# Kernel tuning notes

Hardware: AMD Instinct MI355X
Metric: run time of the kernel (lower is better)

The kernel has to match this reference:

```python
import jax, jax.numpy as jnp
import numpy as np

B, S, N, F, E, EF, H, L = 4, 16, 2048, 32, 16384, 8, 64, 2
H2 = H // 2


def setup_inputs() -> dict:
    key = jax.random.key(0)
    ks = iter(jax.random.split(key, 40))

    def g(shape, s=0.05):
        return jax.random.normal(next(ks), shape, jnp.float32) * s

    return dict(
        x=jax.random.normal(next(ks), (B, S, N, F), jnp.float32),
        edge_index=jax.random.randint(next(ks), (2, E), 0, N, dtype=jnp.int32),
        edge_attr=jax.random.normal(next(ks), (E, EF), jnp.float32),
        Wp=g((F, H)), bp=jnp.zeros((H,), jnp.float32),
        Wl=g((L, H, H)), bl=jnp.zeros((L, H), jnp.float32),
        Wr=g((L, H, H)), br=jnp.zeros((L, H), jnp.float32),
        We=g((L, EF, H)), att=g((L, H)), gb=jnp.zeros((L, H), jnp.float32),
        Wih=g((L, 3 * H, H)), Whh=g((L, 3 * H, H)),
        bih=jnp.zeros((L, 3 * H), jnp.float32), bhh=jnp.zeros((L, 3 * H), jnp.float32),
        oW1=g((H, H2)), ob1=jnp.zeros((H2,), jnp.float32),
        oW2=g((H2, 1)), ob2=jnp.zeros((1,), jnp.float32),
        dW1=g((H, H2)), db1=jnp.zeros((H2,), jnp.float32),
        dW2=g((H2, 1)), db2=jnp.zeros((1,), jnp.float32),
    )


def reference(x, edge_index, edge_attr, Wp, bp, Wl, bl, Wr, br, We, att, gb,
              Wih, Whh, bih, bhh, oW1, ob1, oW2, ob2, dW1, db1, dW2, db2):
    b, s, n, f = x.shape
    nl, _, h = Wl.shape
    src, dst = edge_index[0], edge_index[1]
    # GATv2Conv add_self_loops with fill_value='mean': self-loop attr = mean of
    # incoming edge attrs per destination node (0 if none).
    ones = jnp.ones((src.shape[0],), x.dtype)
    cnt = jax.ops.segment_sum(ones, dst, num_segments=n)
    loop_attr = jax.ops.segment_sum(edge_attr, dst, num_segments=n) / jnp.maximum(cnt, 1.0)[:, None]
    ar = jnp.arange(n, dtype=src.dtype)
    src_f = jnp.concatenate([src, ar])
    dst_f = jnp.concatenate([dst, ar])
    ea_f = jnp.concatenate([edge_attr, loop_attr], axis=0)  # [E2, EF]

    def gat(Xg, l):
        # Xg: [G, N, H] -- GATv2 (heads=1) applied independently per graph.
        XL = Xg @ Wl[l] + bl[l]
        XR = Xg @ Wr[l] + br[l]
        ep = ea_f @ We[l]                              # [E2, H]
        m = XL[:, src_f] + XR[:, dst_f] + ep[None]     # [G, E2, H]
        m = jax.nn.leaky_relu(m, 0.2)
        logits = m @ att[l]                            # [G, E2]
        seg_max = jax.vmap(lambda lg: jax.ops.segment_max(lg, dst_f, num_segments=n))(logits)
        p = jnp.exp(logits - seg_max[:, dst_f])
        den = jax.vmap(lambda pg: jax.ops.segment_sum(pg, dst_f, num_segments=n))(p)
        alpha = p / den[:, dst_f]
        out = jax.vmap(lambda a, xl: jax.ops.segment_sum(a[:, None] * xl[src_f], dst_f, num_segments=n))(alpha, XL)
        return out + gb[l]

    def gru(seq, l):
        # seq: [T, M, H]; PyTorch GRU gate order (r, z, n), scan over T.
        def step(hprev, xt):
            gi = xt @ Wih[l].T + bih[l]
            gh = hprev @ Whh[l].T + bhh[l]
            ir, iz, inn = jnp.split(gi, 3, -1)
            hr, hz, hn = jnp.split(gh, 3, -1)
            r = jax.nn.sigmoid(ir + hr)
            z = jax.nn.sigmoid(iz + hz)
            nn_ = jnp.tanh(inn + r * hn)
            hnew = (1.0 - z) * nn_ + z * hprev
            return hnew, hnew
        h0 = jnp.zeros(seq.shape[1:], seq.dtype)
        _, ys = jax.lax.scan(step, h0, seq)
        return ys

    X = x @ Wp + bp  # [B, S, N, H]
    for l in range(nl):
        # Original code applies GAT per (outer-t, inner-b) pair; the inner
        # TemporalGNN's GRU recurs over the BATCH axis (length B) per outer t.
        hg = gat(X.reshape(b * s, n, h), l).reshape(b, s, n, h)
        X = gru(hg.reshape(b, s * n, h), l).reshape(b, s, n, h)
    xl = X[:, -1].reshape(b * n, h)  # x[:, -1] then per-node heads, concat dim=1
    order = jax.nn.relu(xl @ oW1 + ob1) @ oW2 + ob2
    demand = jax.nn.relu(xl @ dW1 + db1) @ dW2 + db2
    return order[None], demand[None]  # each [1, B*N, 1]
```

## Files before the change

kernel.cpp:

```cpp
#include <hip/hip_runtime.h>
#include <math.h>

#define Bb   4
#define Ss   16
#define Nn   2048
#define Ff   32
#define Ee   16384
#define EFf  8
#define Hh   64
#define HB2  32
#define E2c  (Ee + Nn)
#define RTOT (Bb*Ss*Nn)
#define Mm   (Ss*Nn)
#define CST  68

typedef __attribute__((ext_vector_type(8))) short short8;
typedef __attribute__((ext_vector_type(4))) float f32x4;
#define MFMA16 __builtin_amdgcn_mfma_f32_16x16x32_bf16

__device__ __forceinline__ float sigf(float x) { return 1.f / (1.f + __expf(-x)); }
__device__ __forceinline__ float tanhfast(float x) { return 2.f / (1.f + __expf(-2.f * x)) - 1.f; }

__device__ __forceinline__ void split_bf16(float x, unsigned short& h, unsigned short& l) {
  unsigned u = __float_as_uint(x);
  unsigned r = (u + 0x7FFFu + ((u >> 16) & 1u)) >> 16;
  h = (unsigned short)r;
  float rest = x - __uint_as_float(r << 16);
  unsigned u2 = __float_as_uint(rest);
  l = (unsigned short)((u2 + 0x7FFFu + ((u2 >> 16) & 1u)) >> 16);
}

template <int PAT>
__device__ __forceinline__ float xorf(float v) {
  return __int_as_float(__builtin_amdgcn_ds_swizzle(__float_as_int(v), PAT));
}
__device__ __forceinline__ float red8(float v) {
  int x = __builtin_amdgcn_update_dpp(0, __float_as_int(v), 0x128, 0xF, 0xF, true);
  v += __int_as_float(x);
  v += xorf<0x401F>(v);
  v += __shfl_xor(v, 32, 64);
  return v;
}
__device__ __forceinline__ float redlogit(float v) {
  int x;
  x = __builtin_amdgcn_update_dpp(0, __float_as_int(v), 0xB1, 0xF, 0xF, true);
  v += __int_as_float(x);
  x = __builtin_amdgcn_update_dpp(0, __float_as_int(v), 0x4E, 0xF, 0xF, true);
  v += __int_as_float(x);
  v += xorf<0x101F>(v);
  return v;
}

__global__ __launch_bounds__(256) void k_loop_accum(
    const int* __restrict__ ei, const float* __restrict__ ea,
    float* __restrict__ cntF, float* __restrict__ loopA) {
  int idx = blockIdx.x * 256 + threadIdx.x;
  int e = idx >> 3, j = idx & 7;
  int d = ei[Ee + e];
  atomicAdd(&loopA[d * EFf + j], ea[idx]);
  if (j == 0) atomicAdd(&cntF[d], 1.0f);
}

__global__ __launch_bounds__(256) void k_scan(
    const float* __restrict__ cntF, int* __restrict__ offs) {
  __shared__ int partial[256];
  int tid = threadIdx.x;
  int base = tid * 8;
  int vals[8];
  int s = 0;
  for (int i = 0; i < 8; ++i) {
    int c = (int)cntF[base + i] + 1;
    vals[i] = c;
    s += c;
  }
  partial[tid] = s;
  __syncthreads();
  for (int off = 1; off < 256; off <<= 1) {
    int v = partial[tid];
    int add = (tid >= off) ? partial[tid - off] : 0;
    __syncthreads();
    partial[tid] = v + add;
    __syncthreads();
  }
  int run = (tid == 0) ? 0 : partial[tid - 1];
  for (int i = 0; i < 8; ++i) {
    offs[base + i] = run;
    run += vals[i];
  }
  if (tid == 255) offs[Nn] = run;
}

__global__ __launch_bounds__(256) void k_scatter(
    const int* __restrict__ ei, const int* __restrict__ offs,
    int* __restrict__ fillI, int* __restrict__ posOf, int* __restrict__ srcA) {
  int e = blockIdx.x * 256 + threadIdx.x;
  if (e >= E2c) return;
  int d = (e < Ee) ? ei[Ee + e] : (e - Ee);
  int s = (e < Ee) ? ei[e]      : (e - Ee);
  int pos = offs[d] + atomicAdd(&fillI[d], 1);
  posOf[e] = pos;
  srcA[pos] = s;
}

__global__ __launch_bounds__(256) void k_wprep(
    const float* __restrict__ Wl, const float* __restrict__ Wr,
    const float* __restrict__ Wih, const float* __restrict__ Whh,
    unsigned short* __restrict__ WXhi, unsigned short* __restrict__ WXlo,
    unsigned short* __restrict__ WGhi, unsigned short* __restrict__ WGlo) {
  int idx = blockIdx.x * 256 + threadIdx.x;
  if (idx < 16384) {
    int j = idx & 7, lane = (idx >> 3) & 63, kh = (idx >> 9) & 1;
    int t = (idx >> 10) & 7, l = idx >> 13;
    int n = t * 16 + (lane & 15);
    int k = kh * 32 + ((lane >> 4) << 3) + j;
    const float* W = (n < 64) ? (Wl + (size_t)l * 4096) : (Wr + (size_t)l * 4096);
    float v = W[k * 64 + (n & 63)];
    unsigned short h, lo;
    split_bf16(v, h, lo);
    WXhi[idx] = h; WXlo[idx] = lo;
  } else {
    int i2 = idx - 16384;
    int j = i2 & 7, lane = (i2 >> 3) & 63, kh = (i2 >> 9) & 1;
    int t = (i2 >> 10) % 24, l = i2 / 24576;
    int n = t * 16 + (lane & 15);
    int k = kh * 32 + ((lane >> 4) << 3) + j;
    int g = n >> 6, c = n & 63;
    const float* W = (g < 3) ? (Wih + (size_t)l * 12288 + (size_t)(g * 64 + c) * 64)
                             : (Whh + (size_t)l * 12288 + (size_t)((g - 3) * 64 + c) * 64);
    float v = W[k];
    unsigned short h, lo;
    split_bf16(v, h, lo);
    WGhi[i2] = h; WGlo[i2] = lo;
  }
}

__global__ __launch_bounds__(256) void k_ep(
    const float* __restrict__ ea, const float* __restrict__ loopA,
    const float* __restrict__ We, const int* __restrict__ posOf,
    const float* __restrict__ cntF, float* __restrict__ EPc) {
  __shared__ float wlds[EFf * Hh];
  int tid = threadIdx.x;
  int l = blockIdx.y;
  const float* Wel = We + (size_t)l * EFf * Hh;
  if (tid < EFf * Hh) wlds[tid] = Wel[tid];
  if (tid + 256 < EFf * Hh) wlds[tid + 256] = Wel[tid + 256];
  __syncthreads();
  int idx = blockIdx.x * 256 + tid;
  int e = idx >> 6, j = idx & 63;
  const float* a = (e < Ee) ? (ea + (size_t)e * EFf) : (loopA + (size_t)(e - Ee) * EFf);
  float acc = 0.f;
#pragma unroll
  for (int k = 0; k < EFf; ++k) acc += a[k] * wlds[k * Hh + j];
  if (e >= Ee) acc /= fmaxf(cntF[e - Ee], 1.0f);
  EPc[(size_t)l * E2c * Hh + (((size_t)posOf[e]) << 6) + j] = acc;
}

__global__ __launch_bounds__(256) void k_proj(
    const float* __restrict__ X, const float* __restrict__ Wp,
    const float* __restrict__ bp, float* __restrict__ Out) {
  __shared__ float w[32 * 16];
  int tid = threadIdx.x;
  int j0 = blockIdx.y << 4;
  for (int idx = tid; idx < 32 * 16; idx += 256)
    w[idx] = Wp[((idx >> 4) << 6) + j0 + (idx & 15)];
  __syncthreads();
  int r0 = (blockIdx.x << 9) + tid;
  float acc[2][16];
#pragma unroll
  for (int jj = 0; jj < 16; ++jj) { float b = bp[j0 + jj]; acc[0][jj] = b; acc[1][jj] = b; }
  const float* x0 = X + ((size_t)r0 << 5);
  const float* x1 = x0 + (256 << 5);
  for (int kc = 0; kc < 8; ++kc) {
    float4 a0 = *(const float4*)(x0 + 4 * kc);
    float4 a1 = *(const float4*)(x1 + 4 * kc);
    float a0a[4] = {a0.x, a0.y, a0.z, a0.w};
    float a1a[4] = {a1.x, a1.y, a1.z, a1.w};
#pragma unroll
    for (int q = 0; q < 4; ++q) {
      const float4* wp4 = (const float4*)(w + ((4 * kc + q) << 4));
#pragma unroll
      for (int q4 = 0; q4 < 4; ++q4) {
        float4 wv = wp4[q4];
        acc[0][4*q4+0] = fmaf(a0a[q], wv.x, acc[0][4*q4+0]);
        acc[0][4*q4+1] = fmaf(a0a[q], wv.y, acc[0][4*q4+1]);
        acc[0][4*q4+2] = fmaf(a0a[q], wv.z, acc[0][4*q4+2]);
        acc[0][4*q4+3] = fmaf(a0a[q], wv.w, acc[0][4*q4+3]);
        acc[1][4*q4+0] = fmaf(a1a[q], wv.x, acc[1][4*q4+0]);
        acc[1][4*q4+1] = fmaf(a1a[q], wv.y, acc[1][4*q4+1]);
        acc[1][4*q4+2] = fmaf(a1a[q], wv.z, acc[1][4*q4+2]);
        acc[1][4*q4+3] = fmaf(a1a[q], wv.w, acc[1][4*q4+3]);
      }
    }
  }
#pragma unroll
  for (int rr = 0; rr < 2; ++rr) {
    float* op = Out + (((size_t)(r0 + 256 * rr)) << 6) + j0;
#pragma unroll
    for (int q4 = 0; q4 < 4; ++q4)
      *(float4*)(op + 4 * q4) = make_float4(acc[rr][4*q4], acc[rr][4*q4+1], acc[rr][4*q4+2], acc[rr][4*q4+3]);
  }
}

__global__ __launch_bounds__(256) void k_xlr_mm(
    const float* __restrict__ X,
    const unsigned short* __restrict__ WXhi, const unsigned short* __restrict__ WXlo,
    const float* __restrict__ bl_, const float* __restrict__ br_,
    float* __restrict__ XL, float* __restrict__ XR) {
  __shared__ unsigned short ahi[4096], alo[4096];
  __shared__ float cbuf[64 * CST];
  int tid = threadIdx.x, lane = tid & 63, wv = tid >> 6;
  size_t m0 = (size_t)blockIdx.x << 6;
#pragma unroll
  for (int it = 0; it < 2; ++it) {
    int task = (it << 8) + tid;
    int row = task >> 3, cOct = task & 7;
    const float* src = X + ((m0 + row) << 6) + (cOct << 3);
    float4 a = *(const float4*)src;
    float4 b = *(const float4*)(src + 4);
    float va[8] = {a.x, a.y, a.z, a.w, b.x, b.y, b.z, b.w};
    short8 hv, lv;
#pragma unroll
    for (int j = 0; j < 8; ++j) {
      unsigned short hs, ls;
      split_bf16(va[j], hs, ls);
      hv[j] = (short)hs; lv[j] = (short)ls;
    }
    int f = ((cOct >> 2) * 4 + (row >> 4)) * 64 + ((cOct & 3) << 4) + (row & 15);
    *(short8*)&ahi[f << 3] = hv;
    *(short8*)&alo[f << 3] = lv;
  }
  __syncthreads();
  short8 Ah0 = *(const short8*)&ahi[((0 + wv) << 6 | lane) << 3];
  short8 Al0 = *(const short8*)&alo[((0 + wv) << 6 | lane) << 3];
  short8 Ah1 = *(const short8*)&ahi[((4 + wv) << 6 | lane) << 3];
  short8 Al1 = *(const short8*)&alo[((4 + wv) << 6 | lane) << 3];
  int nl = lane & 15;
  f32x4 acc[8];
#pragma unroll
  for (int t = 0; t < 8; ++t) {
    int n = t * 16 + nl;
    float b = (n < 64) ? bl_[n] : br_[n - 64];
    acc[t] = (f32x4){b, b, b, b};
  }
#pragma unroll
  for (int t = 0; t < 8; ++t) {
    const short8* bh0p = (const short8*)(WXhi + ((t << 1) << 9)) + lane;
    const short8* bl0p = (const short8*)(WXlo + ((t << 1) << 9)) + lane;
    const short8* bh1p = (const short8*)(WXhi + (((t << 1) + 1) << 9)) + lane;
    const short8* bl1p = (const short8*)(WXlo + (((t << 1) + 1) << 9)) + lane;
    short8 bh0 = *bh0p, bl0 = *bl0p, bh1 = *bh1p, bl1 = *bl1p;
    acc[t] = MFMA16(Ah0, bh0, acc[t], 0, 0, 0);
    acc[t] = MFMA16(Ah0, bl0, acc[t], 0, 0, 0);
    acc[t] = MFMA16(Al0, bh0, acc[t], 0, 0, 0);
    acc[t] = MFMA16(Ah1, bh1, acc[t], 0, 0, 0);
    acc[t] = MFMA16(Ah1, bl1, acc[t], 0, 0, 0);
    acc[t] = MFMA16(Al1, bh1, acc[t], 0, 0, 0);
  }
  int rbase = (wv << 4) + ((lane >> 4) << 2);
#pragma unroll
  for (int half = 0; half < 2; ++half) {
    __syncthreads();
#pragma unroll
    for (int tt = 0; tt < 4; ++tt) {
      int t = (half << 2) + tt;
#pragma unroll
      for (int reg = 0; reg < 4; ++reg)
        cbuf[(rbase + reg) * CST + (tt << 4) + nl] = acc[t][reg];
    }
    __syncthreads();
    float* dst = half ? XR : XL;
#pragma unroll
    for (int i = 0; i < 4; ++i) {
      int idx = (i << 10) + (tid << 2);
      int row = idx >> 6, col = idx & 63;
      *(float4*)(dst + ((m0 + row) << 6) + col) = *(float4*)&cbuf[row * CST + col];
    }
  }
}

__global__ __launch_bounds__(256) void k_gat(
    const float* __restrict__ XL, float* __restrict__ XR_HG,
    const float* __restrict__ EPc, const int* __restrict__ offs,
    const int* __restrict__ srcA,
    const float* __restrict__ att, const float* __restrict__ gbl) {
  int d = blockIdx.x;
  int q = blockIdx.y;
  int tid = threadIdx.x;
  int wv = tid >> 6, lane = tid & 63;
  int eSub = lane >> 3, hOct = lane & 7;
  int hb = hOct << 3;
  float at[8], gv[8];
  {
    float4 a0 = *(const float4*)(att + hb);
    float4 a1 = *(const float4*)(att + hb + 4);
    float4 g0v = *(const float4*)(gbl + hb);
    float4 g1v = *(const float4*)(gbl + hb + 4);
    at[0]=a0.x; at[1]=a0.y; at[2]=a0.z; at[3]=a0.w;
    at[4]=a1.x; at[5]=a1.y; at[6]=a1.z; at[7]=a1.w;
    gv[0]=g0v.x; gv[1]=g0v.y; gv[2]=g0v.z; gv[3]=g0v.w;
    gv[4]=g1v.x; gv[5]=g1v.y; gv[6]=g1v.z; gv[7]=g1v.w;
  }
  int p0 = offs[d], p1 = offs[d + 1];
  int nE = p1 - p0;
  int nCh = (nE + 7) >> 3;
  int gbase = (q << 4) + wv;
  size_t rowg[4];
  const float* Xg[4];
  float xr[4][8];
#pragma unroll
  for (int c = 0; c < 4; ++c) {
    int g = gbase + (c << 2);
    rowg[c] = ((size_t)(g * Nn + d)) << 6;
    Xg[c] = XL + (((size_t)g * Nn) << 6);
    float4 a = *(const float4*)(XR_HG + rowg[c] + hb);
    float4 b = *(const float4*)(XR_HG + rowg[c] + hb + 4);
    xr[c][0]=a.x; xr[c][1]=a.y; xr[c][2]=a.z; xr[c][3]=a.w;
    xr[c][4]=b.x; xr[c][5]=b.y; xr[c][6]=b.z; xr[c][7]=b.w;
  }
  float Sd[4] = {0.f, 0.f, 0.f, 0.f};
  float acc[4][8];
#pragma unroll
  for (int c = 0; c < 4; ++c)
#pragma unroll
    for (int j = 0; j < 8; ++j) acc[c][j] = 0.f;

  for (int ck = 0; ck < nCh; ++ck) {
    int p = (ck << 3) + eSub;
    int pc = p < nE ? p : nE - 1;
    int s = srcA[p0 + pc];
    const float* epp = EPc + (((size_t)(p0 + pc)) << 6) + hb;
    float4 e0 = *(const float4*)epp;
    float4 e1 = *(const float4*)(epp + 4);
    float ep[8] = {e0.x, e0.y, e0.z, e0.w, e1.x, e1.y, e1.z, e1.w};
    float xlv[4][8];
#pragma unroll
    for (int c = 0; c < 4; ++c) {
      const float* xp = Xg[c] + ((size_t)s << 6) + hb;
      float4 x0 = *(const float4*)xp;
      float4 x1 = *(const float4*)(xp + 4);
      xlv[c][0]=x0.x; xlv[c][1]=x0.y; xlv[c][2]=x0.z; xlv[c][3]=x0.w;
      xlv[c][4]=x1.x; xlv[c][5]=x1.y; xlv[c][6]=x1.z; xlv[c][7]=x1.w;
    }
    float v[4] = {0.f, 0.f, 0.f, 0.f};
#pragma unroll
    for (int c = 0; c < 4; ++c)
#pragma unroll
      for (int j = 0; j < 8; ++j) {
        float m = xlv[c][j] + xr[c][j] + ep[j];
        m = fmaxf(m, 0.2f * m);
        v[c] = fmaf(m, at[j], v[c]);
      }
#pragma unroll
    for (int c = 0; c < 4; ++c) v[c] = redlogit(v[c]);
    bool live = (p < nE);
#pragma unroll
    for (int c = 0; c < 4; ++c) {
      float w = live ? __expf(v[c]) : 0.f;
      Sd[c] += w;
#pragma unroll
      for (int j = 0; j < 8; ++j) acc[c][j] = fmaf(w, xlv[c][j], acc[c][j]);
    }
  }
#pragma unroll
  for (int c = 0; c < 4; ++c) {
    Sd[c] = red8(Sd[c]);
#pragma unroll
    for (int j = 0; j < 8; ++j) acc[c][j] = red8(acc[c][j]);
  }
  if (eSub == 0) {
#pragma unroll
    for (int c = 0; c < 4; ++c) {
      float inv = 1.f / Sd[c];
      float* op = XR_HG + rowg[c] + hb;
      *(float4*)(op)     = make_float4(fmaf(acc[c][0], inv, gv[0]), fmaf(acc[c][1], inv, gv[1]),
                                       fmaf(acc[c][2], inv, gv[2]), fmaf(acc[c][3], inv, gv[3]));
      *(float4*)(op + 4) = make_float4(fmaf(acc[c][4], inv, gv[4]), fmaf(acc[c][5], inv, gv[5]),
                                       fmaf(acc[c][6], inv, gv[6]), fmaf(acc[c][7], inv, gv[7]));
    }
  }
}

__device__ __forceinline__ void mm6(f32x4& acc,
    short8 Ah0, short8 Al0, short8 Ah1, short8 Al1,
    const unsigned short* __restrict__ Whi, const unsigned short* __restrict__ Wlo,
    int tt, int lane) {
  const short8* bh0p = (const short8*)(Whi + (tt << 10)) + lane;
  const short8* bl0p = (const short8*)(Wlo + (tt << 10)) + lane;
  const short8* bh1p = (const short8*)(Whi + (tt << 10) + 512) + lane;
  const short8* bl1p = (const short8*)(Wlo + (tt << 10) + 512) + lane;
  short8 bh0 = *bh0p, bl0 = *bl0p, bh1 = *bh1p, bl1 = *bl1p;
  acc = MFMA16(Ah0, bh0, acc, 0, 0, 0);
  acc = MFMA16(Ah0, bl0, acc, 0, 0, 0);
  acc = MFMA16(Al0, bh0, acc, 0, 0, 0);
  acc = MFMA16(Ah1, bh1, acc, 0, 0, 0);
  acc = MFMA16(Ah1, bl1, acc, 0, 0, 0);
  acc = MFMA16(Al1, bh1, acc, 0, 0, 0);
}

__global__ __launch_bounds__(256) void k_gru_fused(
    const float* __restrict__ hgAll,
    const unsigned short* __restrict__ WGhi, const unsigned short* __restrict__ WGlo,
    const float* __restrict__ bih, const float* __restrict__ bhh,
    float* __restrict__ houtAll) {
  __shared__ unsigned short ghi[4096], glo[4096], phi[4096], plo[4096];
  __shared__ float cbuf[64 * CST];
  int tid = threadIdx.x, lane = tid & 63, wv = tid >> 6;
  int nl = lane & 15;
  int rbase = (wv << 4) + ((lane >> 4) << 2);
  size_t m0 = (size_t)blockIdx.x << 6;

  float biasR[4], biasZ[4], biasN[4], biasH[4];
#pragma unroll
  for (int ct = 0; ct < 4; ++ct) {
    int c = (ct << 4) + nl;
    biasR[ct] = bih[c]       + bhh[c];
    biasZ[ct] = bih[64 + c]  + bhh[64 + c];
    biasN[ct] = bih[128 + c];
    biasH[ct] = bhh[128 + c];
  }
  float hreg[4][4];
#pragma unroll
  for (int ct = 0; ct < 4; ++ct)
#pragma unroll
    for (int r = 0; r < 4; ++r) hreg[ct][r] = 0.f;

  float4 pa[2], pb[2];
#pragma unroll
  for (int it = 0; it < 2; ++it) {
    int task = (it << 8) + tid;
    int row = task >> 3, cOct = task & 7;
    const float* srcg = hgAll + ((m0 + row) << 6) + (cOct << 3);
    pa[it] = *(const float4*)srcg;
    pb[it] = *(const float4*)(srcg + 4);
  }

  for (int t = 0; t < Bb; ++t) {
#pragma unroll
    for (int it = 0; it < 2; ++it) {
      int task = (it << 8) + tid;
      int row = task >> 3, cOct = task & 7;
      float va[8] = {pa[it].x, pa[it].y, pa[it].z, pa[it].w,
                     pb[it].x, pb[it].y, pb[it].z, pb[it].w};
      short8 hv8, lv8;
#pragma unroll
      for (int j = 0; j < 8; ++j) {
        unsigned short hs, ls;
        split_bf16(va[j], hs, ls);
        hv8[j] = (short)hs; lv8[j] = (short)ls;
      }
      int f = ((cOct >> 2) * 4 + (row >> 4)) * 64 + ((cOct & 3) << 4) + (row & 15);
      *(short8*)&ghi[f << 3] = hv8;
      *(short8*)&glo[f << 3] = lv8;
    }
    __syncthreads();

    short8 Gh0 = *(const short8*)&ghi[((0 + wv) << 6 | lane) << 3];
    short8 Gl0 = *(const short8*)&glo[((0 + wv) << 6 | lane) << 3];
    short8 Gh1 = *(const short8*)&ghi[((4 + wv) << 6 | lane) << 3];
    short8 Gl1 = *(const short8*)&glo[((4 + wv) << 6 | lane) << 3];

    if (t + 1 < Bb) {
      const float* hg = hgAll + (size_t)(t + 1) * ((size_t)Mm * Hh);
#pragma unroll
      for (int it = 0; it < 2; ++it) {
        int task = (it << 8) + tid;
        int row = task >> 3, cOct = task & 7;
        const float* srcg = hg + ((m0 + row) << 6) + (cOct << 3);
        pa[it] = *(const float4*)srcg;
        pb[it] = *(const float4*)(srcg + 4);
      }
    }

    f32x4 accR[4], accZ[4], accN[4], accH[4];
#pragma unroll
    for (int ct = 0; ct < 4; ++ct) {
      accR[ct] = (f32x4){biasR[ct], biasR[ct], biasR[ct], biasR[ct]};
      accZ[ct] = (f32x4){biasZ[ct], biasZ[ct], biasZ[ct], biasZ[ct]};
      accN[ct] = (f32x4){biasN[ct], biasN[ct], biasN[ct], biasN[ct]};
      accH[ct] = (f32x4){biasH[ct], biasH[ct], biasH[ct], biasH[ct]};
    }
#pragma unroll
    for (int ct = 0; ct < 4; ++ct) {
      mm6(accR[ct], Gh0, Gl0, Gh1, Gl1, WGhi, WGlo, 0 + ct, lane);
      mm6(accZ[ct], Gh0, Gl0, Gh1, Gl1, WGhi, WGlo, 4 + ct, lane);
      mm6(accN[ct], Gh0, Gl0, Gh1, Gl1, WGhi, WGlo, 8 + ct, lane);
    }
    if (t) {
      short8 Ph0 = *(const short8*)&phi[((0 + wv) << 6 | lane) << 3];
      short8 Pl0 = *(const short8*)&plo[((0 + wv) << 6 | lane) << 3];
      short8 Ph1 = *(const short8*)&phi[((4 + wv) << 6 | lane) << 3];
      short8 Pl1 = *(const short8*)&plo[((4 + wv) << 6 | lane) << 3];
#pragma unroll
      for (int ct = 0; ct < 4; ++ct) {
        mm6(accR[ct], Ph0, Pl0, Ph1, Pl1, WGhi, WGlo, 12 + ct, lane);
        mm6(accZ[ct], Ph0, Pl0, Ph1, Pl1, WGhi, WGlo, 16 + ct, lane);
        mm6(accH[ct], Ph0, Pl0, Ph1, Pl1, WGhi, WGlo, 20 + ct, lane);
      }
    }

#pragma unroll
    for (int ct = 0; ct < 4; ++ct) {
#pragma unroll
      for (int r = 0; r < 4; ++r) {
        float rg = sigf(accR[ct][r]);
        float zg = sigf(accZ[ct][r]);
        float ng = tanhfast(accN[ct][r] + rg * accH[ct][r]);
        float h = (1.f - zg) * ng + zg * hreg[ct][r];
        hreg[ct][r] = h;
        cbuf[(rbase + r) * CST + (ct << 4) + nl] = h;
      }
    }
    __syncthreads();

    float* hout = houtAll + (size_t)t * ((size_t)Mm * Hh);
#pragma unroll
    for (int i = 0; i < 4; ++i) {
      int idx = (i << 10) + (tid << 2);
      int row = idx >> 6, col = idx & 63;
      *(float4*)(hout + ((m0 + row) << 6) + col) = *(float4*)&cbuf[row * CST + col];
    }
    if (t + 1 < Bb) {
#pragma unroll
      for (int it = 0; it < 2; ++it) {
        int task = (it << 8) + tid;
        int row = task >> 3, cOct = task & 7;
        const float* srcp = &cbuf[row * CST + (cOct << 3)];
        short8 hv8, lv8;
#pragma unroll
        for (int j = 0; j < 8; ++j) {
          unsigned short hs, ls;
          split_bf16(srcp[j], hs, ls);
          hv8[j] = (short)hs; lv8[j] = (short)ls;
        }
        int f = ((cOct >> 2) * 4 + (row >> 4)) * 64 + ((cOct & 3) << 4) + (row & 15);
        *(short8*)&phi[f << 3] = hv8;
        *(short8*)&plo[f << 3] = lv8;
      }
    }
  }
}

__global__ __launch_bounds__(256) void k_heads(
    const float* __restrict__ Xb,
    const float* __restrict__ oW1, const float* __restrict__ ob1,
    const float* __restrict__ oW2, const float* __restrict__ ob2,
    const float* __restrict__ dW1, const float* __restrict__ db1,
    const float* __restrict__ dW2, const float* __restrict__ db2,
    float* __restrict__ out) {
  __shared__ float xa[64 * 65];
  __shared__ float w1o[64 * 32], w1d[64 * 32];
  __shared__ float po[4][64], pd[4][64];
  int tid = threadIdx.x;
  int rblk = blockIdx.x << 6;
  int b = rblk >> 11;
  int n0 = rblk & (Nn - 1);
  const float* src = Xb + (((size_t)b * Ss + (Ss - 1)) * Nn + n0) * Hh;
#pragma unroll
  for (int i = 0; i < 4; ++i) {
    int idx = (i << 10) + (tid << 2);
    int row = idx >> 6, col = idx & 63;
    float4 v = *(const float4*)(src + idx);
    float* dp = &xa[row * 65 + col];
    dp[0] = v.x; dp[1] = v.y; dp[2] = v.z; dp[3] = v.w;
  }
  for (int idx = tid; idx < 2048; idx += 256) {
    w1o[idx] = oW1[idx];
    w1d[idx] = dW1[idx];
  }
  __syncthreads();
  int row = tid & 63;
  int jg = tid >> 6;
  int j0 = jg << 3;
  float hO[8], hD[8];
#pragma unroll
  for (int j = 0; j < 8; ++j) { hO[j] = ob1[j0 + j]; hD[j] = db1[j0 + j]; }
  const float* xr = &xa[row * 65];
  for (int k = 0; k < 64; ++k) {
    float xv = xr[k];
    const float4* wo = (const float4*)&w1o[(k << 5) + j0];
    const float4* wd = (const float4*)&w1d[(k << 5) + j0];
    float4 o0 = wo[0], o1 = wo[1], d0 = wd[0], d1 = wd[1];
    hO[0] = fmaf(xv, o0.x, hO[0]); hO[1] = fmaf(xv, o0.y, hO[1]);
    hO[2] = fmaf(xv, o0.z, hO[2]); hO[3] = fmaf(xv, o0.w, hO[3]);
    hO[4] = fmaf(xv, o1.x, hO[4]); hO[5] = fmaf(xv, o1.y, hO[5]);
    hO[6] = fmaf(xv, o1.z, hO[6]); hO[7] = fmaf(xv, o1.w, hO[7]);
    hD[0] = fmaf(xv, d0.x, hD[0]); hD[1] = fmaf(xv, d0.y, hD[1]);
    hD[2] = fmaf(xv, d0.z, hD[2]); hD[3] = fmaf(xv, d0.w, hD[3]);
    hD[4] = fmaf(xv, d1.x, hD[4]); hD[5] = fmaf(xv, d1.y, hD[5]);
    hD[6] = fmaf(xv, d1.z, hD[6]); hD[7] = fmaf(xv, d1.w, hD[7]);
  }
  float accoP = 0.f, accdP = 0.f;
#pragma unroll
  for (int j = 0; j < 8; ++j) {
    accoP = fmaf(fmaxf(hO[j], 0.f), oW2[j0 + j], accoP);
    accdP = fmaf(fmaxf(hD[j], 0.f), dW2[j0 + j], accdP);
  }
  po[jg][row] = accoP;
  pd[jg][row] = accdP;
  __syncthreads();
  if (tid < 64) {
    int r = rblk + tid;
    out[r]           = ob2[0] + ((po[0][tid] + po[1][tid]) + (po[2][tid] + po[3][tid]));
    out[Bb * Nn + r] = db2[0] + ((pd[0][tid] + pd[1][tid]) + (pd[2][tid] + pd[3][tid]));
  }
}

extern "C" void kernel_launch(void* const* d_in, const int* in_sizes, int n_in,
                              void* d_out, int out_size, void* d_ws, size_t ws_size,
                              hipStream_t stream) {
  const float* x   = (const float*)d_in[0];
  const int*   ei  = (const int*)d_in[1];
  const float* ea  = (const float*)d_in[2];
  const float* Wp  = (const float*)d_in[3];
  const float* bp  = (const float*)d_in[4];
  const float* Wl  = (const float*)d_in[5];
  const float* bl  = (const float*)d_in[6];
  const float* Wr  = (const float*)d_in[7];
  const float* br  = (const float*)d_in[8];
  const float* We  = (const float*)d_in[9];
  const float* att = (const float*)d_in[10];
  const float* gb  = (const float*)d_in[11];
  const float* Wih = (const float*)d_in[12];
  const float* Whh = (const float*)d_in[13];
  const float* bih = (const float*)d_in[14];
  const float* bhh = (const float*)d_in[15];
  const float* oW1 = (const float*)d_in[16];
  const float* ob1 = (const float*)d_in[17];
  const float* oW2 = (const float*)d_in[18];
  const float* ob2 = (const float*)d_in[19];
  const float* dW1 = (const float*)d_in[20];
  const float* db1 = (const float*)d_in[21];
  const float* dW2 = (const float*)d_in[22];
  const float* db2 = (const float*)d_in[23];
  float* out = (float*)d_out;

  float* f    = (float*)d_ws;
  float* Xb   = f;
  float* XLb  = Xb  + (size_t)RTOT * Hh;
  float* XRb  = XLb + (size_t)RTOT * Hh;
  float* EPc  = XRb + (size_t)RTOT * Hh;
  unsigned short* WXhi = (unsigned short*)(EPc + (size_t)2 * E2c * Hh);
  unsigned short* WXlo = WXhi + 16384;
  unsigned short* WGhi = WXlo + 16384;
  unsigned short* WGlo = WGhi + 49152;
  float* cntF = (float*)(WGlo + 49152);
  float* loopA = cntF + Nn;
  int*   fillI = (int*)(loopA + Nn * EFf);
  int*   offs  = fillI + Nn;
  int*   posOf = offs + 2052;
  int*   srcA  = posOf + E2c;

  hipMemsetAsync(cntF, 0, (size_t)(Nn + Nn * EFf + Nn) * 4, stream);

  k_loop_accum<<<dim3(Ee * EFf / 256), 256, 0, stream>>>(ei, ea, cntF, loopA);
  k_scan<<<1, 256, 0, stream>>>(cntF, offs);
  k_scatter<<<dim3((E2c + 255) / 256), 256, 0, stream>>>(ei, offs, fillI, posOf, srcA);
  k_wprep<<<dim3(256), 256, 0, stream>>>(Wl, Wr, Wih, Whh, WXhi, WXlo, WGhi, WGlo);

  k_proj<<<dim3(RTOT / 512, 4), 256, 0, stream>>>(x, Wp, bp, Xb);

  k_ep<<<dim3(E2c * Hh / 256, 2), 256, 0, stream>>>(ea, loopA, We, posOf, cntF, EPc);

  for (int l = 0; l < 2; ++l) {
    k_xlr_mm<<<dim3(RTOT / 64), 256, 0, stream>>>(
        Xb, WXhi + (size_t)l * 8192, WXlo + (size_t)l * 8192,
        bl + (size_t)l * Hh, br + (size_t)l * Hh, XLb, XRb);
    k_gat<<<dim3(Nn, 4), 256, 0, stream>>>(
        XLb, XRb, EPc + (size_t)l * E2c * Hh, offs, srcA,
        att + (size_t)l * Hh, gb + (size_t)l * Hh);
    k_gru_fused<<<dim3(Mm / 64), 256, 0, stream>>>(
        XRb, WGhi + (size_t)l * 24576, WGlo + (size_t)l * 24576,
        bih + (size_t)l * 192, bhh + (size_t)l * 192, Xb);
  }

  k_heads<<<dim3(Bb * Nn / 64), 256, 0, stream>>>(
      Xb, oW1, ob1, oW2, ob2, dW1, db1, dW2, db2, out);
}
```

Before: 444.5 us.

## Stage GRU weights in LDS and build recurrent MFMA fragments from cbuf directly

The fused GRU kernel now copies all hi/lo bf16 split weights (about 96 KB) into shared memory once per block, so the MFMA B-operands come from LDS instead of global or L2 loads. It drops the separate phi/plo staging pass: each lane reads its previous-hidden fragment straight from cbuf and splits it to bf16 hi/lo in registers. The hidden state is kept in cbuf instead of hreg registers. The large LDS footprint (over 100 KB per block) may cut occupancy to one block per CU, and the per-block weight load adds a startup cost.

```diff
diff --git a/kernel.cpp b/kernel.cpp
--- a/kernel.cpp
+++ b/kernel.cpp
@@ -380,9 +380,9 @@
   }
 }
 
-__device__ __forceinline__ void mm6(f32x4& acc,
+__device__ __forceinline__ void mm6l(f32x4& acc,
     short8 Ah0, short8 Al0, short8 Ah1, short8 Al1,
-    const unsigned short* __restrict__ Whi, const unsigned short* __restrict__ Wlo,
+    const unsigned short* Whi, const unsigned short* Wlo,
     int tt, int lane) {
   const short8* bh0p = (const short8*)(Whi + (tt << 10)) + lane;
   const short8* bl0p = (const short8*)(Wlo + (tt << 10)) + lane;
@@ -402,12 +402,20 @@
     const unsigned short* __restrict__ WGhi, const unsigned short* __restrict__ WGlo,
     const float* __restrict__ bih, const float* __restrict__ bhh,
     float* __restrict__ houtAll) {
-  __shared__ unsigned short ghi[4096], glo[4096], phi[4096], plo[4096];
+  __shared__ unsigned short whi[24576], wlo[24576];
+  __shared__ unsigned short ghi[4096], glo[4096];
   __shared__ float cbuf[64 * CST];
   int tid = threadIdx.x, lane = tid & 63, wv = tid >> 6;
   int nl = lane & 15;
   int rbase = (wv << 4) + ((lane >> 4) << 2);
   size_t m0 = (size_t)blockIdx.x << 6;
+
+#pragma unroll
+  for (int i = 0; i < 12; ++i) {
+    int c = (i << 8) + tid;
+    *(short8*)&whi[c << 3] = *(const short8*)(WGhi + ((size_t)c << 3));
+    *(short8*)&wlo[c << 3] = *(const short8*)(WGlo + ((size_t)c << 3));
+  }
 
   float biasR[4], biasZ[4], biasN[4], biasH[4];
 #pragma unroll
@@ -418,11 +426,6 @@
     biasN[ct] = bih[128 + c];
     biasH[ct] = bhh[128 + c];
   }
-  float hreg[4][4];
-#pragma unroll
-  for (int ct = 0; ct < 4; ++ct)
-#pragma unroll
-    for (int r = 0; r < 4; ++r) hreg[ct][r] = 0.f;
 
   float4 pa[2], pb[2];
 #pragma unroll
@@ -471,6 +474,25 @@
       }
     }
 
+    short8 Ph0{}, Pl0{}, Ph1{}, Pl1{};
+    if (t) {
+      const float* cb = &cbuf[((wv << 4) + (lane & 15)) * CST + ((lane >> 4) << 3)];
+      float4 p00 = *(const float4*)cb;
+      float4 p01 = *(const float4*)(cb + 4);
+      float4 p10 = *(const float4*)(cb + 32);
+      float4 p11 = *(const float4*)(cb + 36);
+      float v0[8] = {p00.x, p00.y, p00.z, p00.w, p01.x, p01.y, p01.z, p01.w};
+      float v1[8] = {p10.x, p10.y, p10.z, p10.w, p11.x, p11.y, p11.z, p11.w};
+#pragma unroll
+      for (int j = 0; j < 8; ++j) {
+        unsigned short hs, ls;
+        split_bf16(v0[j], hs, ls);
+        Ph0[j] = (short)hs; Pl0[j] = (short)ls;
+        split_bf16(v1[j], hs, ls);
+        Ph1[j] = (short)hs; Pl1[j] = (short)ls;
+      }
+    }
+
     f32x4 accR[4], accZ[4], accN[4], accH[4];
 #pragma unroll
     for (int ct = 0; ct < 4; ++ct) {
@@ -481,20 +503,16 @@
     }
 #pragma unroll
     for (int ct = 0; ct < 4; ++ct) {
-      mm6(accR[ct], Gh0, Gl0, Gh1, Gl1, WGhi, WGlo, 0 + ct, lane);
-      mm6(accZ[ct], Gh0, Gl0, Gh1, Gl1, WGhi, WGlo, 4 + ct, lane);
-      mm6(accN[ct], Gh0, Gl0, Gh1, Gl1, WGhi, WGlo, 8 + ct, lane);
+      mm6l(accR[ct], Gh0, Gl0, Gh1, Gl1, whi, wlo, 0 + ct, lane);
+      mm6l(accZ[ct], Gh0, Gl0, Gh1, Gl1, whi, wlo, 4 + ct, lane);
+      mm6l(accN[ct], Gh0, Gl0, Gh1, Gl1, whi, wlo, 8 + ct, lane);
     }
     if (t) {
-      short8 Ph0 = *(const short8*)&phi[((0 + wv) << 6 | lane) << 3];
-      short8 Pl0 = *(const short8*)&plo[((0 + wv) << 6 | lane) << 3];
-      short8 Ph1 = *(const short8*)&phi[((4 + wv) << 6 | lane) << 3];
-      short8 Pl1 = *(const short8*)&plo[((4 + wv) << 6 | lane) << 3];
 #pragma unroll
       for (int ct = 0; ct < 4; ++ct) {
-        mm6(accR[ct], Ph0, Pl0, Ph1, Pl1, WGhi, WGlo, 12 + ct, lane);
-        mm6(accZ[ct], Ph0, Pl0, Ph1, Pl1, WGhi, WGlo, 16 + ct, lane);
-        mm6(accH[ct], Ph0, Pl0, Ph1, Pl1, WGhi, WGlo, 20 + ct, lane);
+        mm6l(accR[ct], Ph0, Pl0, Ph1, Pl1, whi, wlo, 12 + ct, lane);
+        mm6l(accZ[ct], Ph0, Pl0, Ph1, Pl1, whi, wlo, 16 + ct, lane);
+        mm6l(accH[ct], Ph0, Pl0, Ph1, Pl1, whi, wlo, 20 + ct, lane);
       }
     }
 
@@ -502,12 +520,12 @@
     for (int ct = 0; ct < 4; ++ct) {
 #pragma unroll
       for (int r = 0; r < 4; ++r) {
-        float rg = sigf(accR[ct][r]);
+        float rgate = sigf(accR[ct][r]);
         float zg = sigf(accZ[ct][r]);
-        float ng = tanhfast(accN[ct][r] + rg * accH[ct][r]);
-        float h = (1.f - zg) * ng + zg * hreg[ct][r];
-        hreg[ct][r] = h;
-        cbuf[(rbase + r) * CST + (ct << 4) + nl] = h;
+        float ng = tanhfast(accN[ct][r] + rgate * accH[ct][r]);
+        int ci = (rbase + r) * CST + (ct << 4) + nl;
+        float hp = t ? cbuf[ci] : 0.f;
+        cbuf[ci] = (1.f - zg) * ng + zg * hp;
       }
     }
     __syncthreads();
@@ -518,24 +536,6 @@
       int idx = (i << 10) + (tid << 2);
       int row = idx >> 6, col = idx & 63;
       *(float4*)(hout + ((m0 + row) << 6) + col) = *(float4*)&cbuf[row * CST + col];
-    }
-    if (t + 1 < Bb) {
-#pragma unroll
-      for (int it = 0; it < 2; ++it) {
-        int task = (it << 8) + tid;
-        int row = task >> 3, cOct = task & 7;
-        const float* srcp = &cbuf[row * CST + (cOct << 3)];
-        short8 hv8, lv8;
-#pragma unroll
-        for (int j = 0; j < 8; ++j) {
-          unsigned short hs, ls;
-          split_bf16(srcp[j], hs, ls);
-          hv8[j] = (short)hs; lv8[j] = (short)ls;
-        }
-        int f = ((cOct >> 2) * 4 + (row >> 4)) * 64 + ((cOct & 3) << 4) + (row & 15);
-        *(short8*)&phi[f << 3] = hv8;
-        *(short8*)&plo[f << 3] = lv8;
-      }
     }
   }
 }
```

Measured after the change: 395.7 us. -11.0%, faster.
